# Optimization experiments

Measured on AMD Instinct MI355X. Metric: run time of the kernel, lower is better.

## Reference

```python
import jax, jax.numpy as jnp
from jax import lax
import numpy as np

KAPPA_S = 6.0
KAPPA_D = 5.0
POLICY_STRETCH = 2.0
VALUE_STRETCH = 1.0 / 32.0
VALUE_GAUGE = 0.2

RAW_PATTERNS = [
    [[0, 0, 0, 0, -5, 1, 1, 1, 1], [0, 0, 0, 0, -5, -5, -5, -5, -5], 0],
    [[0, 0, 0, 1, -5, 1, 1, 1, 0], [0, 0, 0, -5, -5, -5, -5, -5, 0], 0],
    [[0, 0, 1, 1, -5, 1, 1, 0, 0], [0, 0, -5, -5, -5, -5, -5, 0, 0], 0],
    [[0, 1, 1, 1, -5, 1, 0, 0, 0], [0, -5, -5, -5, -5, -5, 0, 0, 0], 0],
    [[1, 1, 1, 1, -5, 0, 0, 0, 0], [-5, -5, -5, -5, -5, 0, 0, 0, 0], 0],
    [[0, -5, 1, 1, 1, 1, 1, -5, 0], [0, 0, -5, -5, -5, -5, -5, 0, 0], -4],
]


def _all_3xnxn(p3):
    # Lay a 9-long 1D pattern (one per input channel) along the 4 line
    # directions (horizontal, vertical, two diagonals) of a 9x9 kernel.
    f = np.zeros((9, 9, 3, 4), np.float32)
    for ch in range(3):
        v = np.asarray(p3[ch], np.float32)
        f[4, :, ch, 0] = v                       # horizontal
        f[:, 4, ch, 1] = v                       # vertical
        for i in range(9):
            f[i, i, ch, 2] = v[i]                # main diagonal
            f[i, 8 - i, ch, 3] = v[i]            # anti diagonal
    return f


def _assemble_filters():
    # select_patterns: channel 0 -> [offense, defense, defense]; channel 1 -> [defense, offense, defense]
    patterns = []
    for off, de, bias in RAW_PATTERNS:
        patterns.append(([off, de, de], bias))
        patterns.append(([de, off, de], bias))
    filt = np.stack([_all_3xnxn(p) for p, _ in patterns], axis=3)  # (9,9,3,12,4)
    filt = np.reshape(filt, (9, 9, 3, -1))                          # filter idx = 4*pattern + direction
    biases = np.asarray([b for _, b in patterns for _ in range(4)], np.float32)
    return jnp.asarray(filt), jnp.asarray(biases)


def _safe_pow(x, p):
    # x >= 0 everywhere it is used; guards the grad of x**p (p<1) at x==0.
    pos = x > 0
    return jnp.where(pos, jnp.where(pos, x, 1.0) ** p, 0.0)


def setup_inputs() -> dict:
    key = jax.random.key(0)
    state = jax.random.normal(key, (4096, 19, 19, 3), dtype=jnp.float32)
    W, b = _assemble_filters()
    return {"state": state, "W": W, "b": b}


def reference(state, W, b):
    # detector: Conv2D 9x9, 48 filters, SAME padding, relu
    counts = jax.nn.relu(
        lax.conv_general_dilated(
            state, W, window_strides=(1, 1), padding="SAME",
            dimension_numbers=("NHWC", "HWIO", "NHWC"),
        ) + b
    )  # [B, N, N, 48]
    # peel: 3x3 conv with identity-center kernel, VALID padding == crop of 1
    core = counts[:, 1:-1, 1:-1, :]  # [B, N-2, N-2, 48]
    B, H, Wd, _ = core.shape
    # filter index = 8*shift + 4*channel + direction for the 40 line filters
    core40 = core[..., :40].reshape(B, H, Wd, 5, 2, 4)  # (shift, channel, direction)
    s = jnp.sum(core40 ** KAPPA_S, axis=3)               # sum over shifts -> [B,H,W,2,4]
    sd = jnp.sum(_safe_pow(s, KAPPA_D / KAPPA_S), axis=4)  # sum over directions -> [B,H,W,2]
    f = _safe_pow(sd, 1.0 / KAPPA_D)                     # [B,H,W,2]; [...,c] = field(channel c)
    f_cur, f_oth = f[..., 0], f[..., 1]
    logits = (f_cur + f_oth).reshape(B, -1)
    probs = jax.nn.softmax(POLICY_STRETCH * logits, axis=-1)
    raw_value = VALUE_GAUGE * (jnp.sum(f_cur, axis=(1, 2)) - jnp.sum(f_oth, axis=(1, 2)))
    value = jnp.tanh(VALUE_STRETCH * raw_value)
    return probs, value
```

## Files before the change

kernel.cpp:

```cpp
#include <hip/hip_runtime.h>
#include <math.h>


__device__ __forceinline__ float fpow(float x, float e) {
    float r = __builtin_amdgcn_exp2f(e * __builtin_amdgcn_logf(x));
    return (x > 0.f) ? r : 0.f;
}
__device__ __forceinline__ float fexp(float x) {
    return __builtin_amdgcn_exp2f(x * 1.44269504088896f);
}

#define F2_E   0
#define F2_C   729
#define F2_GH  1018
#define F2_GV  1375
#define F2_GD  1732
#define F2_GA  2458
#define F2_DUMMY 3151
#define F2_TOTAL 3152

__global__ __launch_bounds__(320) void topo_policy_value(
    const float* __restrict__ state,
    float* __restrict__ probs,
    float* __restrict__ value)
{
    __shared__ float2 l2[F2_TOTAL];
    __shared__ float red[16];

    const int tid = threadIdx.x;
    const int b = blockIdx.x;

    #pragma unroll
    for (int i = 0; i < 3; ++i) {
        int idx = tid + i * 320;
        if (idx < 729) l2[idx] = make_float2(0.f, 0.f);
    }
    __syncthreads();

    const float* src = state + (size_t)b * (19 * 19 * 3);
    for (int j = tid; j < 361; j += 320) {
        int br = j / 19, bc = j - br * 19;
        float l0 = src[3 * j], l1 = src[3 * j + 1], l2v = src[3 * j + 2];
        float e0 = fmaf(-5.f, l1 + l2v, l0);
        float e1 = fmaf(-5.f, l0 + l2v, l1);
        l2[F2_E + (br + 4) * 27 + (bc + 4)] = make_float2(e0, e1);
        if (br >= 1 && br <= 17 && bc >= 1 && bc <= 17) {
            l2[F2_C + (br - 1) * 17 + (bc - 1)] = make_float2(6.f * l0, 6.f * l1);
        }
    }
    __syncthreads();

    if (tid < 100) {
        int t = tid, L;
        int base, step, outp, cnt;
        if (t < 17) {
            L = t;
            base = (L + 5) * 27 + 1; step = 1;
            outp = F2_GH + L * 21; cnt = 21;
        } else if (t < 34) {
            L = t - 17;
            base = 27 + (L + 5); step = 27;
            outp = F2_GV + L * 21; cnt = 21;
        } else if (t < 67) {
            L = t - 34;
            int d = L - 16;
            int j0 = (d < 0) ? -d : 0;
            base = (j0 + 1 + d) * 27 + (j0 + 1); step = 28;
            outp = F2_GD + L * 22 + j0;
            cnt = 21 - ((d < 0) ? -d : d);
        } else {
            L = t - 67;
            int k0 = (L > 16) ? (L - 16) : 0;
            int k1 = (L + 4 < 20) ? (L + 4) : 20;
            base = 26 * k0 + 36 + L; step = 26;
            outp = F2_GA + L * 21 + k0;
            cnt = k1 - k0 + 1;
        }
        float2 buf[5];
        #pragma unroll
        for (int i = 0; i < 5; ++i) buf[i] = l2[base + i * step];
        float sx = buf[0].x + buf[1].x + buf[2].x + buf[3].x + buf[4].x;
        float sy = buf[0].y + buf[1].y + buf[2].y + buf[3].y + buf[4].y;
        #pragma unroll
        for (int i = 0; i < 21; ++i) {
            int dst = (i < cnt) ? (outp + i) : F2_DUMMY;
            l2[dst] = make_float2(sx, sy);
            float2 nc = l2[base + (i + 5) * step];
            float2 oc = buf[i % 5];
            sx += nc.x - oc.x;
            sy += nc.y - oc.y;
            buf[i % 5] = nc;
        }
    }
    __syncthreads();

    const bool act = tid < 289;
    float fcur = 0.f, foth = 0.f;
    if (act) {
        const int y = tid / 17;
        const int x = tid - y * 17;
        const float2 h = l2[F2_C + tid];

        const int bh = F2_GH + y * 21 + x;
        const int bv = F2_GV + x * 21 + y;
        const int bd = F2_GD + (y - x + 16) * 22 + x;
        const int ba = F2_GA + (y + x) * 21 + y;

        float sd0 = 0.f, sd1 = 0.f;
        #define ORIENT(B)                                             \
        {                                                             \
            float t0 = 0.f, t1 = 0.f;                                 \
            _Pragma("unroll")                                         \
            for (int i = 0; i < 5; ++i) {                             \
                float2 w = l2[(B) + i];                               \
                float a0 = fmaxf(w.x - h.x, 0.f);                     \
                float a1 = fmaxf(w.y - h.y, 0.f);                     \
                float q0 = a0 * a0, q1 = a1 * a1;                     \
                float m0 = q0 * q0, m1 = q1 * q1;                     \
                t0 = fmaf(m0, q0, t0); t1 = fmaf(m1, q1, t1);         \
            }                                                         \
            sd0 += fpow(t0, 5.0f / 6.0f);                             \
            sd1 += fpow(t1, 5.0f / 6.0f);                             \
        }
        ORIENT(bh)
        ORIENT(bv)
        ORIENT(bd)
        ORIENT(ba)
        #undef ORIENT

        fcur = fpow(sd0, 0.2f);
        foth = fpow(sd1, 0.2f);
    }

    const float g = act ? 2.f * (fcur + foth) : -3.0e38f;
    float lmax = g;
    float ldif = fcur - foth;

    #pragma unroll
    for (int off = 32; off > 0; off >>= 1) {
        lmax = fmaxf(lmax, __shfl_down(lmax, off, 64));
        ldif += __shfl_down(ldif, off, 64);
    }
    const int wave = tid >> 6;
    if ((tid & 63) == 0) { red[wave] = lmax; red[5 + wave] = ldif; }
    __syncthreads();
    if (tid == 0) {
        float m = red[0];
        #pragma unroll
        for (int w = 1; w < 5; ++w) m = fmaxf(m, red[w]);
        red[15] = m;
        red[14] = red[5] + red[6] + red[7] + red[8] + red[9];
    }
    __syncthreads();

    const float M = red[15];
    const float e = act ? fexp(g - M) : 0.f;
    float lsum = e;
    #pragma unroll
    for (int off = 32; off > 0; off >>= 1) lsum += __shfl_down(lsum, off, 64);
    if ((tid & 63) == 0) red[wave] = lsum;
    __syncthreads();
    if (tid == 0) red[13] = red[0] + red[1] + red[2] + red[3] + red[4];
    __syncthreads();

    const float invS = 1.0f / red[13];
    if (act) probs[(size_t)b * 289 + tid] = e * invS;
    if (tid == 0) value[b] = tanhf(red[14] * (0.2f / 32.0f));
}

extern "C" void kernel_launch(void* const* d_in, const int* in_sizes, int n_in,
                              void* d_out, int out_size, void* d_ws, size_t ws_size,
                              hipStream_t stream) {
    const float* state = (const float*)d_in[0];
    const int nb = in_sizes[0] / (19 * 19 * 3);
    float* probs = (float*)d_out;
    float* value = probs + (size_t)nb * 289;
    topo_policy_value<<<dim3(nb), dim3(320), 0, stream>>>(state, probs, value);
}
```

Measured before the change: 85.27 us.

## Process two boards per block and cut reduction barriers

Each block of 640 threads now handles two boards in separate shared-memory slabs, which halves the grid size. The separate zero-fill pass and its barrier are folded into the load loop, which now writes the whole padded 27x27 grid, padding included. In the softmax and value reductions, every thread combines the per-wave partials itself instead of thread 0 doing it between extra barriers, which removes two __syncthreads. The cost is twice the shared memory per block (about 50KB), which may limit how many blocks fit on a CU, and the larger blocks synchronise more threads at each barrier.

```diff
diff --git a/kernel.cpp b/kernel.cpp
--- a/kernel.cpp
+++ b/kernel.cpp
@@ -16,76 +16,87 @@
 #define F2_GV  1375
 #define F2_GD  1732
 #define F2_GA  2458
-#define F2_DUMMY 3151
-#define F2_TOTAL 3152
+#define F2_SLAB 3152
+#define F2_DUMMY 6304
+#define F2_TOTAL 6305
 
-__global__ __launch_bounds__(320) void topo_policy_value(
+__global__ __launch_bounds__(640) void topo_policy_value(
     const float* __restrict__ state,
     float* __restrict__ probs,
-    float* __restrict__ value)
+    float* __restrict__ value,
+    int nb)
 {
     __shared__ float2 l2[F2_TOTAL];
-    __shared__ float red[16];
+    __shared__ float rmax[10], rdif[10], rsum[10];
 
     const int tid = threadIdx.x;
-    const int b = blockIdx.x;
+    const int s   = tid >= 320;
+    const int w   = tid - (s ? 320 : 0);
+    const int sb  = blockIdx.x * 2 + s;
+    const bool vboard = sb < nb;
+    const int base = s ? F2_SLAB : 0;
 
+    const float* src = state + (size_t)sb * (19 * 19 * 3);
     #pragma unroll
-    for (int i = 0; i < 3; ++i) {
-        int idx = tid + i * 320;
-        if (idx < 729) l2[idx] = make_float2(0.f, 0.f);
-    }
-    __syncthreads();
-
-    const float* src = state + (size_t)b * (19 * 19 * 3);
-    for (int j = tid; j < 361; j += 320) {
-        int br = j / 19, bc = j - br * 19;
-        float l0 = src[3 * j], l1 = src[3 * j + 1], l2v = src[3 * j + 2];
-        float e0 = fmaf(-5.f, l1 + l2v, l0);
-        float e1 = fmaf(-5.f, l0 + l2v, l1);
-        l2[F2_E + (br + 4) * 27 + (bc + 4)] = make_float2(e0, e1);
-        if (br >= 1 && br <= 17 && bc >= 1 && bc <= 17) {
-            l2[F2_C + (br - 1) * 17 + (bc - 1)] = make_float2(6.f * l0, 6.f * l1);
+    for (int it = 0; it < 3; ++it) {
+        int j = w + it * 320;
+        if (j < 729) {
+            int py = j / 27, px = j - py * 27;
+            int r = py - 4, c = px - 4;
+            bool in = vboard && (unsigned)r < 19u && (unsigned)c < 19u;
+            float l0 = 0.f, l1 = 0.f, lv2 = 0.f;
+            if (in) {
+                int o = 3 * (r * 19 + c);
+                l0 = src[o]; l1 = src[o + 1]; lv2 = src[o + 2];
+            }
+            float e0 = fmaf(-5.f, l1 + lv2, l0);
+            float e1 = fmaf(-5.f, l0 + lv2, l1);
+            l2[base + F2_E + j] = make_float2(e0, e1);
+            if (r >= 1 && r <= 17 && c >= 1 && c <= 17) {
+                l2[base + F2_C + (r - 1) * 17 + (c - 1)] =
+                    make_float2(6.f * l0, 6.f * l1);
+            }
         }
     }
     __syncthreads();
 
-    if (tid < 100) {
-        int t = tid, L;
-        int base, step, outp, cnt;
+    if (w < 100) {
+        int t = w, L;
+        int gb, step, outp, cnt;
         if (t < 17) {
             L = t;
-            base = (L + 5) * 27 + 1; step = 1;
+            gb = (L + 5) * 27 + 1; step = 1;
             outp = F2_GH + L * 21; cnt = 21;
         } else if (t < 34) {
             L = t - 17;
-            base = 27 + (L + 5); step = 27;
+            gb = 27 + (L + 5); step = 27;
             outp = F2_GV + L * 21; cnt = 21;
         } else if (t < 67) {
             L = t - 34;
             int d = L - 16;
             int j0 = (d < 0) ? -d : 0;
-            base = (j0 + 1 + d) * 27 + (j0 + 1); step = 28;
+            gb = (j0 + 1 + d) * 27 + (j0 + 1); step = 28;
             outp = F2_GD + L * 22 + j0;
             cnt = 21 - ((d < 0) ? -d : d);
         } else {
             L = t - 67;
             int k0 = (L > 16) ? (L - 16) : 0;
             int k1 = (L + 4 < 20) ? (L + 4) : 20;
-            base = 26 * k0 + 36 + L; step = 26;
+            gb = 26 * k0 + 36 + L; step = 26;
             outp = F2_GA + L * 21 + k0;
             cnt = k1 - k0 + 1;
         }
+        gb += base; outp += base;
         float2 buf[5];
         #pragma unroll
-        for (int i = 0; i < 5; ++i) buf[i] = l2[base + i * step];
+        for (int i = 0; i < 5; ++i) buf[i] = l2[gb + i * step];
         float sx = buf[0].x + buf[1].x + buf[2].x + buf[3].x + buf[4].x;
         float sy = buf[0].y + buf[1].y + buf[2].y + buf[3].y + buf[4].y;
         #pragma unroll
         for (int i = 0; i < 21; ++i) {
             int dst = (i < cnt) ? (outp + i) : F2_DUMMY;
             l2[dst] = make_float2(sx, sy);
-            float2 nc = l2[base + (i + 5) * step];
+            float2 nc = l2[gb + (i + 5) * step];
             float2 oc = buf[i % 5];
             sx += nc.x - oc.x;
             sy += nc.y - oc.y;
@@ -94,17 +105,17 @@
     }
     __syncthreads();
 
-    const bool act = tid < 289;
+    const bool act = w < 289;
     float fcur = 0.f, foth = 0.f;
     if (act) {
-        const int y = tid / 17;
-        const int x = tid - y * 17;
-        const float2 h = l2[F2_C + tid];
+        const int y = w / 17;
+        const int x = w - y * 17;
+        const float2 h = l2[base + F2_C + w];
 
-        const int bh = F2_GH + y * 21 + x;
-        const int bv = F2_GV + x * 21 + y;
-        const int bd = F2_GD + (y - x + 16) * 22 + x;
-        const int ba = F2_GA + (y + x) * 21 + y;
+        const int bh = base + F2_GH + y * 21 + x;
+        const int bv = base + F2_GV + x * 21 + y;
+        const int bd = base + F2_GD + (y - x + 16) * 22 + x;
+        const int ba = base + F2_GA + (y + x) * 21 + y;
 
         float sd0 = 0.f, sd1 = 0.f;
         #define ORIENT(B)                                             \
@@ -112,9 +123,9 @@
             float t0 = 0.f, t1 = 0.f;                                 \
             _Pragma("unroll")                                         \
             for (int i = 0; i < 5; ++i) {                             \
-                float2 w = l2[(B) + i];                               \
-                float a0 = fmaxf(w.x - h.x, 0.f);                     \
-                float a1 = fmaxf(w.y - h.y, 0.f);                     \
+                float2 wv = l2[(B) + i];                              \
+                float a0 = fmaxf(wv.x - h.x, 0.f);                    \
+                float a1 = fmaxf(wv.y - h.y, 0.f);                    \
                 float q0 = a0 * a0, q1 = a1 * a1;                     \
                 float m0 = q0 * q0, m1 = q1 * q1;                     \
                 t0 = fmaf(m0, q0, t0); t1 = fmaf(m1, q1, t1);         \
@@ -135,37 +146,34 @@
     const float g = act ? 2.f * (fcur + foth) : -3.0e38f;
     float lmax = g;
     float ldif = fcur - foth;
-
     #pragma unroll
     for (int off = 32; off > 0; off >>= 1) {
         lmax = fmaxf(lmax, __shfl_down(lmax, off, 64));
         ldif += __shfl_down(ldif, off, 64);
     }
-    const int wave = tid >> 6;
-    if ((tid & 63) == 0) { red[wave] = lmax; red[5 + wave] = ldif; }
-    __syncthreads();
-    if (tid == 0) {
-        float m = red[0];
-        #pragma unroll
-        for (int w = 1; w < 5; ++w) m = fmaxf(m, red[w]);
-        red[15] = m;
-        red[14] = red[5] + red[6] + red[7] + red[8] + red[9];
-    }
+    const int wv_id = tid >> 6;
+    if ((tid & 63) == 0) { rmax[wv_id] = lmax; rdif[wv_id] = ldif; }
     __syncthreads();
 
-    const float M = red[15];
+    const int rb = s * 5;
+    float M = rmax[rb];
+    #pragma unroll
+    for (int k = 1; k < 5; ++k) M = fmaxf(M, rmax[rb + k]);
+
     const float e = act ? fexp(g - M) : 0.f;
     float lsum = e;
     #pragma unroll
     for (int off = 32; off > 0; off >>= 1) lsum += __shfl_down(lsum, off, 64);
-    if ((tid & 63) == 0) red[wave] = lsum;
-    __syncthreads();
-    if (tid == 0) red[13] = red[0] + red[1] + red[2] + red[3] + red[4];
+    if ((tid & 63) == 0) rsum[wv_id] = lsum;
     __syncthreads();
 
-    const float invS = 1.0f / red[13];
-    if (act) probs[(size_t)b * 289 + tid] = e * invS;
-    if (tid == 0) value[b] = tanhf(red[14] * (0.2f / 32.0f));
+    float S = rsum[rb] + rsum[rb + 1] + rsum[rb + 2] + rsum[rb + 3] + rsum[rb + 4];
+    const float invS = 1.0f / S;
+    if (vboard && act) probs[(size_t)sb * 289 + w] = e * invS;
+    if (vboard && w == 0) {
+        float D = rdif[rb] + rdif[rb + 1] + rdif[rb + 2] + rdif[rb + 3] + rdif[rb + 4];
+        value[sb] = tanhf(D * (0.2f / 32.0f));
+    }
 }
 
 extern "C" void kernel_launch(void* const* d_in, const int* in_sizes, int n_in,
@@ -175,5 +183,6 @@
     const int nb = in_sizes[0] / (19 * 19 * 3);
     float* probs = (float*)d_out;
     float* value = probs + (size_t)nb * 289;
-    topo_policy_value<<<dim3(nb), dim3(320), 0, stream>>>(state, probs, value);
+    const int grid = (nb + 1) / 2;
+    topo_policy_value<<<dim3(grid), dim3(640), 0, stream>>>(state, probs, value, nb);
 }
```

New measurement: 91.34 us. 7.1% more time.
